# Kernel optimization log

Measured on AMD Instinct MI355X. Metric: run time of the kernel, lower is better.

Reference implementation:

```python
import jax, jax.numpy as jnp
import numpy as np


def setup_inputs() -> dict:
    key = jax.random.key(0)
    ks = jax.random.split(key, 7)
    N = 262144
    Ka, La = 8, 8
    Kb, Lb, Mb = 8, 8, 4
    Kc, Lc, Mc = 8, 8, 4
    return {
        "x": jax.random.normal(ks[0], (N, 2), dtype=jnp.float32),
        "a_real": 0.001 * jax.random.normal(ks[1], (Ka, La), dtype=jnp.float32),
        "a_imag": 0.001 * jax.random.normal(ks[2], (Ka, La), dtype=jnp.float32),
        "b_real": 0.001 * jax.random.normal(ks[3], (Kb, Lb, Mb), dtype=jnp.float32),
        "b_imag": 0.001 * jax.random.normal(ks[4], (Kb, Lb, Mb), dtype=jnp.float32),
        "c_real": 0.001 * jax.random.normal(ks[5], (Kc, Lc, Mc), dtype=jnp.float32),
        "c_imag": 0.001 * jax.random.normal(ks[6], (Kc, Lc, Mc), dtype=jnp.float32),
    }


def _gmp(x, a_real, a_imag, b_real, b_imag, c_real, c_imag):
    # x: (N,2) real I/Q -> complex signal (iq_handler equivalent)
    xc = (x[:, 0] + 1j * x[:, 1]).astype(jnp.complex64)
    a = (a_real + 1j * a_imag).astype(jnp.complex64)   # (Ka,La)
    b = (b_real + 1j * b_imag).astype(jnp.complex64)   # (Kb,Lb,Mb)
    c = (c_real + 1j * c_imag).astype(jnp.complex64)   # (Kc,Lc,Mc)
    N = xc.shape[0]
    Ka, La = a.shape
    Kb, Lb, Mb = b.shape
    Kc, Lc, Mc = c.shape
    n = jnp.arange(N)

    # ---- aligned term (a): delayed taps, power series in |x[n-l]| ----
    idx_La = jnp.clip(n[None, :] - jnp.arange(La)[:, None], 0, N - 1)   # (La,N)
    x_La = xc[idx_La]                                                   # (La,N)
    pow_a = jnp.abs(x_La)[..., None] ** jnp.arange(Ka, dtype=jnp.float32)  # (La,N,Ka)
    term_a = jnp.einsum('kl,ln,lnk->n', a, x_La, pow_a)

    # ---- lagging cross-term (b): envelope delayed by extra m >= 0 ----
    idx_Lb = jnp.clip(n[None, :] - jnp.arange(Lb)[:, None], 0, N - 1)   # (Lb,N)
    x_Lb = xc[idx_Lb]                                                   # (Lb,N)
    idx_Mb = jnp.clip(n[None, None, :] - jnp.arange(Lb)[:, None, None]
                      - jnp.arange(Mb)[None, :, None], 0, N - 1)        # (Lb,Mb,N)
    x_Mb = xc[idx_Mb]                                                   # (Lb,Mb,N)
    pow_b = jnp.abs(x_Mb)[..., None] ** jnp.arange(Kb, dtype=jnp.float32)  # (Lb,Mb,N,Kb)
    term_b = jnp.einsum('klm,ln,lmnk->n', b, x_Lb, pow_b)

    # ---- leading cross-term (c): envelope advanced by m >= 0 ----
    idx_Lc = jnp.clip(n[None, :] - jnp.arange(Lc)[:, None], 0, N - 1)   # (Lc,N)
    x_Lc = xc[idx_Lc]                                                   # (Lc,N)
    idx_Mc = jnp.clip(n[None, None, :] - jnp.arange(Lc)[:, None, None]
                      + jnp.arange(Mc)[None, :, None], 0, N - 1)        # (Lc,Mc,N)
    x_Mc = xc[idx_Mc]                                                   # (Lc,Mc,N)
    pow_c = jnp.abs(x_Mc)[..., None] ** jnp.arange(Kc, dtype=jnp.float32)  # (Lc,Mc,N,Kc)
    term_c = jnp.einsum('klm,ln,lmnk->n', c, x_Lc, pow_c)

    y = term_a + term_b + term_c                                        # (N,) complex
    return jnp.stack([y.real, y.imag], axis=-1)                         # back to I/Q (N,2)


def reference(x, a_real, a_imag, b_real, b_imag, c_real, c_imag):
    return _gmp(x, a_real, a_imag, b_real, b_imag, c_real, c_imag)
```

## Files before the change

kernel.cpp:

```cpp
#include <hip/hip_runtime.h>
#include <type_traits>

typedef float v2f __attribute__((ext_vector_type(2)));

constexpr int BLOCK = 256;
constexpr int SPB = 128;
constexpr int HALO_LO = 10;
constexpr int HALO_HI = 3;
constexpr int SIG = SPB + HALO_LO + HALO_HI;

template<int I, int N, typename F>
__device__ __forceinline__ void unroll_for(F&& f) {
    if constexpr (I < N) {
        f(std::integral_constant<int, I>{});
        unroll_for<I + 1, N>(static_cast<F&&>(f));
    }
}

__global__ __launch_bounds__(BLOCK) void gmp_kernel(
    const float* __restrict__ x,
    const float* __restrict__ a_re, const float* __restrict__ a_im,
    const float* __restrict__ b_re, const float* __restrict__ b_im,
    const float* __restrict__ c_re, const float* __restrict__ c_im,
    float* __restrict__ out, int N)
{
    __shared__ float2 sx[SIG];
    __shared__ float sab[SIG];
    __shared__ float2 part[4][SPB];
    __shared__ __align__(16) float wlds[896];

    const int t = threadIdx.x;
    const int n0 = blockIdx.x * SPB;

    const float2* x2 = (const float2*)x;
    if (t < SIG) {
        int g = n0 - HALO_LO + t;
        g = max(0, min(N - 1, g));
        float2 v = x2[g];
        sx[t] = v;
        sab[t] = __builtin_amdgcn_sqrtf(fmaf(v.x, v.x, v.y * v.y));
    }

    for (int idx = t; idx < 448; idx += BLOCK) {
        int l = idx / 56;
        int rem = idx - l * 56;
        int s = rem >> 3;
        int k = rem & 7;
        int akl = k * 8 + l;
        float re, im;
        if (s == 0) {
            re = a_re[akl] + b_re[akl * 4] + c_re[akl * 4];
            im = a_im[akl] + b_im[akl * 4] + c_im[akl * 4];
        } else if (s <= 3) {
            re = b_re[akl * 4 + s];
            im = b_im[akl * 4 + s];
        } else {
            re = c_re[akl * 4 + (s - 3)];
            im = c_im[akl * 4 + (s - 3)];
        }
        wlds[idx * 2]     = re;
        wlds[idx * 2 + 1] = im;
    }
    __syncthreads();

    const int s2 = t & 63;
    const int wv = __builtin_amdgcn_readfirstlane(t >> 6);
    const float* cw = &wlds[wv * 224];

    const int rb = 2 * s2 + 6 - 2 * wv;
    float rv[9];
    unroll_for<0, 9>([&](auto I) { rv[I.value] = sab[rb + I.value]; });
    float xvr[3], xvi[3];
    unroll_for<0, 3>([&](auto I) {
        float2 v = sx[rb + 3 + I.value];
        xvr[I.value] = v.x;
        xvi[I.value] = v.y;
    });

    float y0r = 0.f, y0i = 0.f, y1r = 0.f, y1i = 0.f;

    unroll_for<0, 2>([&](auto LL) {
        constexpr int ll = LL.value;
        v2f S0 = {0.f, 0.f}, S1 = {0.f, 0.f};
        unroll_for<0, 7>([&](auto Sc) {
            constexpr int s = Sc.value;
            constexpr int d = (s == 0) ? 0 : ((s <= 3) ? -s : (s - 3));
            constexpr int off = ll * 112 + s * 16;
            v2f wk[8];
            unroll_for<0, 8>([&](auto K) {
                wk[K.value] = *(const v2f*)&cw[off + 2 * K.value];
            });
            const float r0 = rv[4 - ll + d];
            const float r1 = rv[5 - ll + d];
            const v2f rr0 = {r0, r0};
            const v2f rr1 = {r1, r1};
            v2f acc0 = wk[7];
            v2f acc1 = acc0;
            unroll_for<0, 7>([&](auto Kc) {
                constexpr int k = 6 - Kc.value;
                acc0 = __builtin_elementwise_fma(acc0, rr0, wk[k]);
                acc1 = __builtin_elementwise_fma(acc1, rr1, wk[k]);
            });
            S0 += acc0;
            S1 += acc1;
        });
        {
            const float xre = xvr[1 - ll], xim = xvi[1 - ll];
            y0r = fmaf(xre, S0.x, fmaf(-xim, S0.y, y0r));
            y0i = fmaf(xre, S0.y, fmaf( xim, S0.x, y0i));
        }
        {
            const float xre = xvr[2 - ll], xim = xvi[2 - ll];
            y1r = fmaf(xre, S1.x, fmaf(-xim, S1.y, y1r));
            y1i = fmaf(xre, S1.y, fmaf( xim, S1.x, y1i));
        }
    });

    part[wv][2 * s2]     = make_float2(y0r, y0i);
    part[wv][2 * s2 + 1] = make_float2(y1r, y1i);
    __syncthreads();

    if (t < SPB) {
        float2 p0 = part[0][t];
        float2 p1 = part[1][t];
        float2 p2 = part[2][t];
        float2 p3 = part[3][t];
        float2 r;
        r.x = (p0.x + p1.x) + (p2.x + p3.x);
        r.y = (p0.y + p1.y) + (p2.y + p3.y);
        const int n = n0 + t;
        if (n < N) ((float2*)out)[n] = r;
    }
}

extern "C" void kernel_launch(void* const* d_in, const int* in_sizes, int n_in,
                              void* d_out, int out_size, void* d_ws, size_t ws_size,
                              hipStream_t stream) {
    const float* x    = (const float*)d_in[0];
    const float* a_re = (const float*)d_in[1];
    const float* a_im = (const float*)d_in[2];
    const float* b_re = (const float*)d_in[3];
    const float* b_im = (const float*)d_in[4];
    const float* c_re = (const float*)d_in[5];
    const float* c_im = (const float*)d_in[6];
    float* out = (float*)d_out;

    int N = in_sizes[0] / 2;
    int grid = (N + SPB - 1) / SPB;
    gmp_kernel<<<grid, BLOCK, 0, stream>>>(x, a_re, a_im, b_re, b_im,
                                           c_re, c_im, out, N);
}
```

Measured before the change: 14.04 us.

## Assign one delay tap per wave, keep weights in registers, loop over chunks

The block grows to 8 waves, one per delay tap l, so each wave can hold its 7x8 complex weights in registers for the whole kernel. Each block walks 4 chunks of 256 samples serially, reloading the signal halo for each chunk. Each thread now computes 4 outputs per chunk, and the eight per-wave partials are reduced through shared memory. This is meant to cut repeated LDS weight loads and block launch overhead. In exchange the grid shrinks to about one block per CU, adds extra barriers per chunk, and leaves the global loads unoverlapped with compute, so there is less latency hiding.

```diff
diff --git a/kernel.cpp b/kernel.cpp
--- a/kernel.cpp
+++ b/kernel.cpp
@@ -3,11 +3,14 @@
 
 typedef float v2f __attribute__((ext_vector_type(2)));
 
-constexpr int BLOCK = 256;
-constexpr int SPB = 128;
+constexpr int BLOCK = 512;
+constexpr int CHUNKS = 4;
+constexpr int SPB = 256;
+constexpr int SPBLK = SPB * CHUNKS;
 constexpr int HALO_LO = 10;
 constexpr int HALO_HI = 3;
 constexpr int SIG = SPB + HALO_LO + HALO_HI;
+constexpr int PSTRIDE = 128;
 
 template<int I, int N, typename F>
 __device__ __forceinline__ void unroll_for(F&& f) {
@@ -17,31 +20,32 @@
     }
 }
 
-__global__ __launch_bounds__(BLOCK) void gmp_kernel(
+__global__ __launch_bounds__(BLOCK, 2) void gmp_kernel(
     const float* __restrict__ x,
     const float* __restrict__ a_re, const float* __restrict__ a_im,
     const float* __restrict__ b_re, const float* __restrict__ b_im,
     const float* __restrict__ c_re, const float* __restrict__ c_im,
     float* __restrict__ out, int N)
 {
-    __shared__ float2 sx[SIG];
-    __shared__ float sab[SIG];
-    __shared__ float2 part[4][SPB];
+    __shared__ float sxr[SIG], sxi[SIG], sab[SIG];
+    __shared__ __align__(16) float2 part[8][SPB];
     __shared__ __align__(16) float wlds[896];
 
     const int t = threadIdx.x;
-    const int n0 = blockIdx.x * SPB;
+    const int blk0 = blockIdx.x * SPBLK;
+    const float2* x2 = (const float2*)x;
 
-    const float2* x2 = (const float2*)x;
     if (t < SIG) {
-        int g = n0 - HALO_LO + t;
+        int g = blk0 - HALO_LO + t;
         g = max(0, min(N - 1, g));
         float2 v = x2[g];
-        sx[t] = v;
+        sxr[t] = v.x;
+        sxi[t] = v.y;
         sab[t] = __builtin_amdgcn_sqrtf(fmaf(v.x, v.x, v.y * v.y));
     }
 
-    for (int idx = t; idx < 448; idx += BLOCK) {
+    if (t < 448) {
+        int idx = t;
         int l = idx / 56;
         int rem = idx - l * 56;
         int s = rem >> 3;
@@ -65,71 +69,94 @@
 
     const int s2 = t & 63;
     const int wv = __builtin_amdgcn_readfirstlane(t >> 6);
-    const float* cw = &wlds[wv * 224];
+    const float* cw = &wlds[wv * 112];
 
-    const int rb = 2 * s2 + 6 - 2 * wv;
-    float rv[9];
-    unroll_for<0, 9>([&](auto I) { rv[I.value] = sab[rb + I.value]; });
-    float xvr[3], xvi[3];
-    unroll_for<0, 3>([&](auto I) {
-        float2 v = sx[rb + 3 + I.value];
-        xvr[I.value] = v.x;
-        xvi[I.value] = v.y;
+    v2f wk[7][8];
+    unroll_for<0, 7>([&](auto Sc) {
+        unroll_for<0, 8>([&](auto K) {
+            wk[Sc.value][K.value] =
+                *(const v2f*)&cw[Sc.value * 16 + 2 * K.value];
+        });
     });
 
-    float y0r = 0.f, y0i = 0.f, y1r = 0.f, y1i = 0.f;
+    const int rb0 = 2 * s2 + 7 - wv;
+    const int rb1 = rb0 + PSTRIDE;
 
-    unroll_for<0, 2>([&](auto LL) {
-        constexpr int ll = LL.value;
-        v2f S0 = {0.f, 0.f}, S1 = {0.f, 0.f};
+    for (int c = 0; c < CHUNKS; ++c) {
+        const int n0 = blk0 + c * SPB;
+
+        if (c > 0) {
+            if (t < SIG) {
+                int g = n0 - HALO_LO + t;
+                g = max(0, min(N - 1, g));
+                float2 v = x2[g];
+                sxr[t] = v.x;
+                sxi[t] = v.y;
+                sab[t] = __builtin_amdgcn_sqrtf(fmaf(v.x, v.x, v.y * v.y));
+            }
+            __syncthreads();
+        }
+
+        float rvA[8], rvB[8];
+        unroll_for<0, 8>([&](auto I) {
+            rvA[I.value] = sab[rb0 + I.value];
+            rvB[I.value] = sab[rb1 + I.value];
+        });
+        float xArr[2], xAri[2], xBrr[2], xBri[2];
+        unroll_for<0, 2>([&](auto Q) {
+            xArr[Q.value] = sxr[rb0 + 3 + Q.value];
+            xAri[Q.value] = sxi[rb0 + 3 + Q.value];
+            xBrr[Q.value] = sxr[rb1 + 3 + Q.value];
+            xBri[Q.value] = sxi[rb1 + 3 + Q.value];
+        });
+
+        v2f S[4] = {{0.f,0.f},{0.f,0.f},{0.f,0.f},{0.f,0.f}};
         unroll_for<0, 7>([&](auto Sc) {
             constexpr int s = Sc.value;
-            constexpr int d = (s == 0) ? 0 : ((s <= 3) ? -s : (s - 3));
-            constexpr int off = ll * 112 + s * 16;
-            v2f wk[8];
-            unroll_for<0, 8>([&](auto K) {
-                wk[K.value] = *(const v2f*)&cw[off + 2 * K.value];
-            });
-            const float r0 = rv[4 - ll + d];
-            const float r1 = rv[5 - ll + d];
-            const v2f rr0 = {r0, r0};
-            const v2f rr1 = {r1, r1};
-            v2f acc0 = wk[7];
-            v2f acc1 = acc0;
+            constexpr int d3 = (s == 0) ? 3 : ((s <= 3) ? (3 - s) : s);
+            const float r0A = rvA[0 + d3];
+            const float r1A = rvA[1 + d3];
+            const float r0B = rvB[0 + d3];
+            const float r1B = rvB[1 + d3];
+            v2f acc0 = wk[s][7], acc1 = acc0, acc2 = acc0, acc3 = acc0;
             unroll_for<0, 7>([&](auto Kc) {
                 constexpr int k = 6 - Kc.value;
-                acc0 = __builtin_elementwise_fma(acc0, rr0, wk[k]);
-                acc1 = __builtin_elementwise_fma(acc1, rr1, wk[k]);
+                acc0 = __builtin_elementwise_fma(acc0, (v2f){r0A, r0A}, wk[s][k]);
+                acc1 = __builtin_elementwise_fma(acc1, (v2f){r1A, r1A}, wk[s][k]);
+                acc2 = __builtin_elementwise_fma(acc2, (v2f){r0B, r0B}, wk[s][k]);
+                acc3 = __builtin_elementwise_fma(acc3, (v2f){r1B, r1B}, wk[s][k]);
             });
-            S0 += acc0;
-            S1 += acc1;
+            S[0] += acc0;
+            S[1] += acc1;
+            S[2] += acc2;
+            S[3] += acc3;
         });
+
         {
-            const float xre = xvr[1 - ll], xim = xvi[1 - ll];
-            y0r = fmaf(xre, S0.x, fmaf(-xim, S0.y, y0r));
-            y0i = fmaf(xre, S0.y, fmaf( xim, S0.x, y0i));
+            float pr0 = xArr[0]*S[0].x - xAri[0]*S[0].y;
+            float pi0 = xArr[0]*S[0].y + xAri[0]*S[0].x;
+            float pr1 = xArr[1]*S[1].x - xAri[1]*S[1].y;
+            float pi1 = xArr[1]*S[1].y + xAri[1]*S[1].x;
+            *(float4*)&part[wv][2 * s2] = make_float4(pr0, pi0, pr1, pi1);
+            float qr0 = xBrr[0]*S[2].x - xBri[0]*S[2].y;
+            float qi0 = xBrr[0]*S[2].y + xBri[0]*S[2].x;
+            float qr1 = xBrr[1]*S[3].x - xBri[1]*S[3].y;
+            float qi1 = xBrr[1]*S[3].y + xBri[1]*S[3].x;
+            *(float4*)&part[wv][2 * s2 + PSTRIDE] = make_float4(qr0, qi0, qr1, qi1);
         }
-        {
-            const float xre = xvr[2 - ll], xim = xvi[2 - ll];
-            y1r = fmaf(xre, S1.x, fmaf(-xim, S1.y, y1r));
-            y1i = fmaf(xre, S1.y, fmaf( xim, S1.x, y1i));
+        __syncthreads();
+
+        if (t < SPB) {
+            float2 p0 = part[0][t], p1 = part[1][t];
+            float2 p2 = part[2][t], p3 = part[3][t];
+            float2 p4 = part[4][t], p5 = part[5][t];
+            float2 p6 = part[6][t], p7 = part[7][t];
+            float2 r;
+            r.x = ((p0.x + p1.x) + (p2.x + p3.x)) + ((p4.x + p5.x) + (p6.x + p7.x));
+            r.y = ((p0.y + p1.y) + (p2.y + p3.y)) + ((p4.y + p5.y) + (p6.y + p7.y));
+            const int n = n0 + t;
+            if (n < N) ((float2*)out)[n] = r;
         }
-    });
-
-    part[wv][2 * s2]     = make_float2(y0r, y0i);
-    part[wv][2 * s2 + 1] = make_float2(y1r, y1i);
-    __syncthreads();
-
-    if (t < SPB) {
-        float2 p0 = part[0][t];
-        float2 p1 = part[1][t];
-        float2 p2 = part[2][t];
-        float2 p3 = part[3][t];
-        float2 r;
-        r.x = (p0.x + p1.x) + (p2.x + p3.x);
-        r.y = (p0.y + p1.y) + (p2.y + p3.y);
-        const int n = n0 + t;
-        if (n < N) ((float2*)out)[n] = r;
     }
 }
 
@@ -146,7 +173,7 @@
     float* out = (float*)d_out;
 
     int N = in_sizes[0] / 2;
-    int grid = (N + SPB - 1) / SPB;
+    int grid = (N + SPBLK - 1) / SPBLK;
     gmp_kernel<<<grid, BLOCK, 0, stream>>>(x, a_re, a_im, b_re, b_im,
                                            c_re, c_im, out, N);
 }
```

Result: faster. 12.80 us (-8.8%).
